# Optimization experiments

Hardware: AMD Instinct MI355X
Metric: run time of the kernel (lower is better)

The kernel has to match this reference:

```python
import jax, jax.numpy as jnp
from jax import lax
import numpy as np

B, L, D = 8, 2048, 512
Q, K = 8, 2048


def setup_inputs() -> dict:
    key = jax.random.key(0)
    kx, kc = jax.random.split(key)
    x = jax.random.normal(kx, (B, L, D), dtype=jnp.float32)
    codebooks = jax.random.normal(kc, (Q, K, D), dtype=jnp.float32)  # Q stacked [K, D] embedding tables
    return {"x": x, "codebooks": codebooks}


def reference(x, codebooks):
    # Residual VQ: at each level, nearest-codeword lookup on the residual.
    # cdist argmin == squared-distance argmin: ||r||^2 - 2 r.c + ||c||^2.
    cb_sq = jnp.sum(codebooks * codebooks, axis=-1)  # [Q, K]

    def step(residual, level):
        cb, cb2 = level  # [K, D], [K]
        r2 = jnp.sum(residual * residual, axis=-1, keepdims=True)  # [B, L, 1]
        dots = jnp.einsum('bld,kd->blk', residual, cb)  # [B, L, K]
        dist2 = r2 - 2.0 * dots + cb2  # [B, L, K]
        idx = jnp.argmin(dist2, axis=-1)  # [B, L]
        quant = cb[idx]  # [B, L, D] gather
        return residual - quant, (idx, quant)

    _, (indices, quants) = lax.scan(step, x, (codebooks, cb_sq))
    quantized = jnp.sum(quants, axis=0)  # [B, L, D]
    indices = jnp.moveaxis(indices, 0, 1)  # [B, Q, L] (torch.stack(dim=1))
    return indices, quantized
```

## Files before the change

kernel.cpp:

```cpp
#include <hip/hip_runtime.h>

#define BB 8
#define LL 2048
#define DD 512
#define QQ 8
#define KK 2048
#define MM (BB*LL)

#define NTILES 16

typedef __attribute__((ext_vector_type(8))) short short8;
typedef __attribute__((ext_vector_type(4))) float f32x4;

#define GLDS(src, dst) __builtin_amdgcn_global_load_lds( \
    (const __attribute__((address_space(1))) void*)(src), \
    (__attribute__((address_space(3))) void*)(dst), 16, 0, 0)

#define BARX()  asm volatile("s_barrier" ::: "memory")
#define WAIT0() asm volatile("s_waitcnt vmcnt(0)" ::: "memory")

__device__ __forceinline__ ushort f2bf(float f) {
    uint u = __float_as_uint(f);
    u += 0x7FFFu + ((u >> 16) & 1u);
    return (ushort)(u >> 16);
}

__global__ __launch_bounds__(256) void cb2_kernel(const float* __restrict__ cb,
                                                  float* __restrict__ cb2) {
    int row  = blockIdx.x * 4 + (threadIdx.x >> 6);
    int lane = threadIdx.x & 63;
    const float* r = cb + (size_t)row * DD + lane * 8;
    float4 a = *(const float4*)r;
    float4 b = *(const float4*)(r + 4);
    float s = a.x*a.x + a.y*a.y + a.z*a.z + a.w*a.w
            + b.x*b.x + b.y*b.y + b.z*b.z + b.w*b.w;
    #pragma unroll
    for (int off = 32; off >= 1; off >>= 1) s += __shfl_xor(s, off);
    if (lane == 0) cb2[row] = s;
}

__global__ __launch_bounds__(256) void bprep_kernel(const float* __restrict__ cbq,
                                                    short8* __restrict__ bh2) {
    const int wid  = threadIdx.x >> 6;
    const int lane = threadIdx.x & 63;
    const int col  = blockIdx.x * 4 + wid;
    const float* src = cbq + (size_t)col * DD + lane * 8;
    float4 v0 = *(const float4*)src;
    float4 v1 = *(const float4*)(src + 4);
    short8 h;
    h[0] = (short)f2bf(v0.x); h[1] = (short)f2bf(v0.y);
    h[2] = (short)f2bf(v0.z); h[3] = (short)f2bf(v0.w);
    h[4] = (short)f2bf(v1.x); h[5] = (short)f2bf(v1.y);
    h[6] = (short)f2bf(v1.z); h[7] = (short)f2bf(v1.w);
    bh2[(size_t)col * 64 + lane] = h;
}

__global__ __launch_bounds__(256) void aprep0_kernel(const float* __restrict__ x,
                                                     float* __restrict__ resid,
                                                     short8* __restrict__ ah) {
    const int wid  = threadIdx.x >> 6;
    const int lane = threadIdx.x & 63;
    const int row  = blockIdx.x * 4 + wid;
    const float* src = x + (size_t)row * DD + lane * 8;
    float4 v0 = *(const float4*)src;
    float4 v1 = *(const float4*)(src + 4);
    float* dst = resid + (size_t)row * DD + lane * 8;
    *(float4*)dst       = v0;
    *(float4*)(dst + 4) = v1;
    short8 h;
    h[0] = (short)f2bf(v0.x); h[1] = (short)f2bf(v0.y);
    h[2] = (short)f2bf(v0.z); h[3] = (short)f2bf(v0.w);
    h[4] = (short)f2bf(v1.x); h[5] = (short)f2bf(v1.y);
    h[6] = (short)f2bf(v1.z); h[7] = (short)f2bf(v1.w);
    ah[(size_t)row * 64 + lane] = h;
}

__global__ __launch_bounds__(512, 2) void gemm_argmin_kernel(
    const short8* __restrict__ ah,
    const short8* __restrict__ bh2,
    const float*  __restrict__ cb2q,
    float*        __restrict__ blockv1,
    uint4*        __restrict__ blockmask,
    float W)
{
    __shared__ char smemc[131072];

    const int id  = blockIdx.x;
    const int xcd = id & 7;
    const int s   = id >> 3;
    const int nt  = s & 7;
    const int mt  = xcd * 8 + (s >> 3);

    const int tid  = threadIdx.x;
    const int wid  = tid >> 6;
    const int lane = tid & 63;
    const int wr   = wid >> 2;
    const int wcn  = wid & 3;
    const int l15  = lane & 15, l4 = lane >> 4;

    f32x4 acc[4][8];
    #pragma unroll
    for (int n = 0; n < 4; n++)
        #pragma unroll
        for (int m = 0; m < 8; m++) acc[n][m] = (f32x4){0.f, 0.f, 0.f, 0.f};

    const char* aSrc = (const char*)ah  + ((size_t)mt << 18);
    const char* bSrc = (const char*)bh2 + ((size_t)nt << 18);

    #define STAGEQ(tt, bufn, p) do { \
        int g_ = (p) * 512 + tid; \
        int rL_ = g_ >> 3, st_ = g_ & 7; \
        int k_ = st_ ^ (rL_ & 7); \
        char* db_ = smemc + (bufn) * 65536 + ((p) * 512 + wid * 64) * 16; \
        GLDS(aSrc + (size_t)rL_ * 1024 + (tt) * 128 + k_ * 16, db_); \
        GLDS(bSrc + (size_t)rL_ * 1024 + (tt) * 128 + k_ * 16, db_ + 32768); \
    } while (0)

    short8 af[4][2], bf[4][2];

    #define LDA(mh) do { \
        _Pragma("unroll") for (int mm = 0; mm < 4; mm++) \
        _Pragma("unroll") for (int ks = 0; ks < 2; ks++) { \
            int rL_ = wr * 128 + ((mh) * 4 + mm) * 16 + l15; \
            int c_ = ks * 4 + l4; \
            af[mm][ks] = *(const short8*)(smemc + ab + rL_ * 128 + ((c_ ^ (rL_ & 7)) << 4)); \
        } } while (0)

    #define LDBALL() do { \
        _Pragma("unroll") for (int nn = 0; nn < 4; nn++) \
        _Pragma("unroll") for (int ks = 0; ks < 2; ks++) { \
            int cL_ = wcn * 64 + nn * 16 + l15; \
            int c_ = ks * 4 + l4; \
            bf[nn][ks] = *(const short8*)(smemc + ab + 32768 + cL_ * 128 + ((c_ ^ (cL_ & 7)) << 4)); \
        } } while (0)

    #define PH(mh) do { \
        __builtin_amdgcn_s_setprio(1); \
        _Pragma("unroll") for (int ks = 0; ks < 2; ks++) \
        _Pragma("unroll") for (int nn = 0; nn < 4; nn++) \
        _Pragma("unroll") for (int mm = 0; mm < 4; mm++) \
            acc[nn][(mh)*4+mm] = __builtin_amdgcn_mfma_f32_16x16x32_bf16( \
                bf[nn][ks], af[mm][ks], acc[nn][(mh)*4+mm], 0, 0, 0); \
        __builtin_amdgcn_s_setprio(0); \
    } while (0)

    STAGEQ(0, 0, 0); STAGEQ(0, 0, 1); STAGEQ(0, 0, 2); STAGEQ(0, 0, 3);
    WAIT0();
    BARX();

    for (int t = 0; t < 8; t++) {
        const uint ab = (uint)(t & 1) * 65536u;
        const int nbuf = (t & 1) ^ 1;
        if (t < 7) { STAGEQ(t + 1, nbuf, 0); STAGEQ(t + 1, nbuf, 1);
                     STAGEQ(t + 1, nbuf, 2); STAGEQ(t + 1, nbuf, 3); }
        LDBALL();
        LDA(0);
        PH(0);
        LDA(1);
        PH(1);
        if (t < 7) WAIT0();
        BARX();
    }

    float* halfmin = (float*)smemc;
    uint2* maskS   = (uint2*)(smemc + 4096);

    f32x4 c2v[4];
    #pragma unroll
    for (int n = 0; n < 4; n++)
        c2v[n] = *(const f32x4*)&cb2q[nt * 256 + wcn * 64 + n * 16 + (l4 << 2)];

    #pragma unroll
    for (int m = 0; m < 8; m++) {
        float v = 3.4e38f;
        #pragma unroll
        for (int n = 0; n < 4; n++)
            #pragma unroll
            for (int r = 0; r < 4; r++)
                v = fminf(v, fmaf(-2.f, acc[n][m][r], c2v[n][r]));
        v = fminf(v, __shfl_xor(v, 16));
        v = fminf(v, __shfl_xor(v, 32));
        if (l4 == 0) halfmin[(wr * 128 + m * 16 + l15) * 4 + wcn] = v;
    }
    __syncthreads();

    #pragma unroll
    for (int m = 0; m < 8; m++) {
        int rL = wr * 128 + m * 16 + l15;
        int pb = wcn & 2;
        float vt = fminf(halfmin[rL * 4 + pb], halfmin[rL * 4 + pb + 1]);
        float thrm = vt + W;
        uint blo = 0, bhi = 0;
        #pragma unroll
        for (int n = 0; n < 4; n++)
            #pragma unroll
            for (int r = 0; r < 4; r++) {
                float d = fmaf(-2.f, acc[n][m][r], c2v[n][r]);
                int bit = n * 16 + (l4 << 2) + r;
                if (d < thrm) { if (bit < 32) blo |= 1u << bit; else bhi |= 1u << (bit - 32); }
            }
        blo |= __shfl_xor(blo, 16); bhi |= __shfl_xor(bhi, 16);
        blo |= __shfl_xor(blo, 32); bhi |= __shfl_xor(bhi, 32);
        if (l4 == 0) maskS[rL * 4 + wcn] = make_uint2(blo, bhi);
    }
    __syncthreads();

    {
        int T = tid >> 8, rL = tid & 255;
        float vt = fminf(halfmin[rL * 4 + T * 2], halfmin[rL * 4 + T * 2 + 1]);
        uint2 lo = maskS[rL * 4 + T * 2], hi = maskS[rL * 4 + T * 2 + 1];
        size_t o = (size_t)(nt * 2 + T) * MM + mt * 256 + rL;
        blockv1[o] = vt;
        blockmask[o] = make_uint4(lo.x, lo.y, hi.x, hi.y);
    }
    #undef STAGEQ
    #undef LDA
    #undef LDBALL
    #undef PH
}

__global__ __launch_bounds__(256) void crru_kernel(
    const float*  __restrict__ blockv1,
    const uint4*  __restrict__ blockmask,
    const float*  __restrict__ cbq,
    const float*  __restrict__ cb2q,
    const float*  __restrict__ xin,
    float*        __restrict__ resid,
    float*        __restrict__ idx_out,
    short8*       __restrict__ ah,
    int q, float W)
{
    __shared__ float rs[4][DD];
    const int wid  = threadIdx.x >> 6;
    const int lane = threadIdx.x & 63;
    const int row  = blockIdx.x * 4 + wid;
    const int grp  = lane >> 4, gl = lane & 15;

    float v1 = 3.4e38f;
    uint4 mk = make_uint4(0, 0, 0, 0);
    if (lane < NTILES) {
        size_t o = (size_t)lane * MM + row;
        v1 = blockv1[o];
        mk = blockmask[o];
    }

    float* rrow = resid + (size_t)row * DD + lane * 8;
    float4 r0 = *(const float4*)rrow;
    float4 r1 = *(const float4*)(rrow + 4);
    *(float4*)&rs[wid][lane * 8]     = r0;
    *(float4*)&rs[wid][lane * 8 + 4] = r1;

    float g1 = v1;
    #pragma unroll
    for (int off = 32; off >= 1; off >>= 1) g1 = fminf(g1, __shfl_xor(g1, off));
    const float thr = g1 + W;

    unsigned long long act = __ballot((lane < NTILES) && (v1 < thr));

    float be = 3.4e38f; int bk = 0x7FFFFFFF;
    const float* rsw = rs[wid];

    auto eval4 = [&](int k0, int k1, int k2, int k3) {
        int kg = (grp == 0) ? k0 : (grp == 1) ? k1 : (grp == 2) ? k2 : k3;
        float d = 0.f;
        if (kg >= 0) {
            const float* cp = cbq + (size_t)kg * DD + gl * 32;
            const float* rp = rsw + gl * 32;
            #pragma unroll
            for (int j = 0; j < 8; j++) {
                float4 c = *(const float4*)(cp + j * 4);
                float4 r = *(const float4*)(rp + j * 4);
                d = fmaf(r.x, c.x, d); d = fmaf(r.y, c.y, d);
                d = fmaf(r.z, c.z, d); d = fmaf(r.w, c.w, d);
            }
        }
        #pragma unroll
        for (int off = 8; off >= 1; off >>= 1) d += __shfl_xor(d, off);
        #pragma unroll
        for (int g = 0; g < 4; g++) {
            float dg = __shfl(d, g * 16);
            int kg2 = (g == 0) ? k0 : (g == 1) ? k1 : (g == 2) ? k2 : k3;
            if (kg2 >= 0) {
                float e = fmaf(-2.f, dg, cb2q[kg2]);
                if (e < be || (e == be && kg2 < bk)) { be = e; bk = kg2; }
            }
        }
    };

    while (act) {
        int tile = __ffsll(act) - 1; act &= act - 1;
        uint m0 = __shfl((int)mk.x, tile), m1 = __shfl((int)mk.y, tile);
        uint m2 = __shfl((int)mk.z, tile), m3 = __shfl((int)mk.w, tile);
        unsigned long long lo = ((unsigned long long)m1 << 32) | m0;
        unsigned long long hi = ((unsigned long long)m3 << 32) | m2;
        int base = tile * 128;
        while (lo | hi) {
            int c0 = -1, c1 = -1, c2 = -1, c3 = -1;
            #define POP1(dst) \
                if (lo) { int b = __ffsll(lo) - 1; lo &= lo - 1; dst = base + b; } \
                else if (hi) { int b = __ffsll(hi) - 1; hi &= hi - 1; dst = base + 64 + b; }
            POP1(c0) POP1(c1) POP1(c2) POP1(c3)
            #undef POP1
            eval4(c0, c1, c2, c3);
        }
    }
    const int winner = bk;

    if (lane == 0) {
        int b = row >> 11, l = row & (LL - 1);
        idx_out[((size_t)b * QQ + q) * LL + l] = (float)winner;
    }

    const float* cw = cbq + (size_t)winner * DD + lane * 8;
    float4 c0 = *(const float4*)cw;
    float4 c1 = *(const float4*)(cw + 4);
    float4 n0 = make_float4(r0.x - c0.x, r0.y - c0.y, r0.z - c0.z, r0.w - c0.w);
    float4 n1 = make_float4(r1.x - c1.x, r1.y - c1.y, r1.z - c1.z, r1.w - c1.w);

    if (q < QQ - 1) {
        *(float4*)rrow       = n0;
        *(float4*)(rrow + 4) = n1;
        short8 h;
        h[0] = (short)f2bf(n0.x); h[1] = (short)f2bf(n0.y);
        h[2] = (short)f2bf(n0.z); h[3] = (short)f2bf(n0.w);
        h[4] = (short)f2bf(n1.x); h[5] = (short)f2bf(n1.y);
        h[6] = (short)f2bf(n1.z); h[7] = (short)f2bf(n1.w);
        ah[(size_t)row * 64 + lane] = h;
    } else {
        const float* xw = xin + (size_t)row * DD + lane * 8;
        float4 x0 = *(const float4*)xw;
        float4 x1 = *(const float4*)(xw + 4);
        *(float4*)rrow       = make_float4(x0.x - n0.x, x0.y - n0.y, x0.z - n0.z, x0.w - n0.w);
        *(float4*)(rrow + 4) = make_float4(x1.x - n1.x, x1.y - n1.y, x1.z - n1.z, x1.w - n1.w);
    }
}

extern "C" void kernel_launch(void* const* d_in, const int* in_sizes, int n_in,
                              void* d_out, int out_size, void* d_ws, size_t ws_size,
                              hipStream_t stream) {
    (void)in_sizes; (void)n_in; (void)out_size; (void)ws_size;
    const float* x  = (const float*)d_in[0];
    const float* cb = (const float*)d_in[1];
    float* out = (float*)d_out;

    float* idx_out = out;
    float* resid   = out + (size_t)BB * QQ * LL;

    char* w = (char*)d_ws;
    float*  cb2       = (float*)(w);
    float*  blockv1   = (float*)(w + 0x10000);
    uint4*  blockmask = (uint4*)(w + 0x110000);
    short8* ah        = (short8*)(w + 0x510000);
    short8* bh2       = (short8*)(w + 0x1510000);

    cb2_kernel<<<QQ * KK / 4, 256, 0, stream>>>(cb, cb2);
    aprep0_kernel<<<MM / 4, 256, 0, stream>>>(x, resid, ah);

    for (int q = 0; q < QQ; q++) {
        const float* cbq = cb + (size_t)q * KK * DD;
        const float* c2q = cb2 + (size_t)q * KK;
        const float W = 2.0f + 0.3f * q;

        bprep_kernel<<<KK / 4, 256, 0, stream>>>(cbq, bh2);

        gemm_argmin_kernel<<<512, 512, 0, stream>>>(ah, bh2, c2q,
                                                    blockv1, blockmask, W);

        crru_kernel<<<MM / 4, 256, 0, stream>>>(blockv1, blockmask, cbq, c2q, x,
                                                resid, idx_out, ah, q, W);
    }
}
```

Measured before the change: 517.1 us.

## Hoist codebook bf16 conversion out of the loop and give each GEMM block two M tiles

The bf16 conversion of all eight codebooks now runs once up front into a larger workspace buffer, instead of one conversion kernel per level. The GEMM/argmin kernel now processes two consecutive 256-row M tiles per block with a continuous double-buffered pipeline across both. It runs the epilogue for the first tile mid-loop, which halves the grid to 256 blocks. This removes per-level launches and may reduce tail and startup cost, at the price of a larger LDS footprint and a longer serial block that needs more workspace.

Measured after the change: 648.6 us. +25.4%, slower.

```diff
diff --git a/kernel.cpp b/kernel.cpp
--- a/kernel.cpp
+++ b/kernel.cpp
@@ -39,12 +39,12 @@
     if (lane == 0) cb2[row] = s;
 }
 
-__global__ __launch_bounds__(256) void bprep_kernel(const float* __restrict__ cbq,
-                                                    short8* __restrict__ bh2) {
+__global__ __launch_bounds__(256) void bprep_kernel(const float* __restrict__ cb,
+                                                    short8* __restrict__ bh2all) {
     const int wid  = threadIdx.x >> 6;
     const int lane = threadIdx.x & 63;
     const int col  = blockIdx.x * 4 + wid;
-    const float* src = cbq + (size_t)col * DD + lane * 8;
+    const float* src = cb + (size_t)col * DD + lane * 8;
     float4 v0 = *(const float4*)src;
     float4 v1 = *(const float4*)(src + 4);
     short8 h;
@@ -52,7 +52,7 @@
     h[2] = (short)f2bf(v0.z); h[3] = (short)f2bf(v0.w);
     h[4] = (short)f2bf(v1.x); h[5] = (short)f2bf(v1.y);
     h[6] = (short)f2bf(v1.z); h[7] = (short)f2bf(v1.w);
-    bh2[(size_t)col * 64 + lane] = h;
+    bh2all[(size_t)col * 64 + lane] = h;
 }
 
 __global__ __launch_bounds__(256) void aprep0_kernel(const float* __restrict__ x,
@@ -77,19 +77,19 @@
 
 __global__ __launch_bounds__(512, 2) void gemm_argmin_kernel(
     const short8* __restrict__ ah,
-    const short8* __restrict__ bh2,
+    const short8* __restrict__ bh2q,
     const float*  __restrict__ cb2q,
     float*        __restrict__ blockv1,
     uint4*        __restrict__ blockmask,
     float W)
 {
-    __shared__ char smemc[131072];
+    __shared__ char smemc[147456];
 
     const int id  = blockIdx.x;
     const int xcd = id & 7;
     const int s   = id >> 3;
     const int nt  = s & 7;
-    const int mt  = xcd * 8 + (s >> 3);
+    const int mt0 = xcd * 8 + (s >> 3) * 2;
 
     const int tid  = threadIdx.x;
     const int wid  = tid >> 6;
@@ -104,16 +104,21 @@
         #pragma unroll
         for (int m = 0; m < 8; m++) acc[n][m] = (f32x4){0.f, 0.f, 0.f, 0.f};
 
-    const char* aSrc = (const char*)ah  + ((size_t)mt << 18);
-    const char* bSrc = (const char*)bh2 + ((size_t)nt << 18);
-
-    #define STAGEQ(tt, bufn, p) do { \
+    const char* aS0  = (const char*)ah + ((size_t)mt0 << 18);
+    const char* aS1  = aS0 + (1 << 18);
+    const char* bSrc = (const char*)bh2q + ((size_t)nt << 18);
+
+    #define STAGEQ(abase, tt, bufn, p) do { \
         int g_ = (p) * 512 + tid; \
         int rL_ = g_ >> 3, st_ = g_ & 7; \
         int k_ = st_ ^ (rL_ & 7); \
         char* db_ = smemc + (bufn) * 65536 + ((p) * 512 + wid * 64) * 16; \
-        GLDS(aSrc + (size_t)rL_ * 1024 + (tt) * 128 + k_ * 16, db_); \
+        GLDS((abase) + (size_t)rL_ * 1024 + (tt) * 128 + k_ * 16, db_); \
         GLDS(bSrc + (size_t)rL_ * 1024 + (tt) * 128 + k_ * 16, db_ + 32768); \
+    } while (0)
+    #define STAGE4(abase, tt, bufn) do { \
+        STAGEQ(abase, tt, bufn, 0); STAGEQ(abase, tt, bufn, 1); \
+        STAGEQ(abase, tt, bufn, 2); STAGEQ(abase, tt, bufn, 3); \
     } while (0)
 
     short8 af[4][2], bf[4][2];
@@ -144,79 +149,87 @@
         __builtin_amdgcn_s_setprio(0); \
     } while (0)
 
-    STAGEQ(0, 0, 0); STAGEQ(0, 0, 1); STAGEQ(0, 0, 2); STAGEQ(0, 0, 3);
+    float* halfmin = (float*)(smemc + 131072);
+    uint2* maskS   = (uint2*)(smemc + 131072 + 4096);
+
+    f32x4 c2v[4];
+    #pragma unroll
+    for (int n = 0; n < 4; n++)
+        c2v[n] = *(const f32x4*)&cb2q[nt * 256 + wcn * 64 + n * 16 + (l4 << 2)];
+
+    #define EPI(mtx) do { \
+        _Pragma("unroll") for (int m = 0; m < 8; m++) { \
+            float v = 3.4e38f; \
+            _Pragma("unroll") for (int n = 0; n < 4; n++) \
+            _Pragma("unroll") for (int r = 0; r < 4; r++) \
+                v = fminf(v, fmaf(-2.f, acc[n][m][r], c2v[n][r])); \
+            v = fminf(v, __shfl_xor(v, 16)); \
+            v = fminf(v, __shfl_xor(v, 32)); \
+            if (l4 == 0) halfmin[(wr * 128 + m * 16 + l15) * 4 + wcn] = v; \
+        } \
+        __syncthreads(); \
+        _Pragma("unroll") for (int m = 0; m < 8; m++) { \
+            int rL = wr * 128 + m * 16 + l15; \
+            int pb = wcn & 2; \
+            float vt = fminf(halfmin[rL * 4 + pb], halfmin[rL * 4 + pb + 1]); \
+            float thrm = vt + W; \
+            uint blo = 0, bhi = 0; \
+            _Pragma("unroll") for (int n = 0; n < 4; n++) \
+            _Pragma("unroll") for (int r = 0; r < 4; r++) { \
+                float d = fmaf(-2.f, acc[n][m][r], c2v[n][r]); \
+                int bit = n * 16 + (l4 << 2) + r; \
+                if (d < thrm) { if (bit < 32) blo |= 1u << bit; else bhi |= 1u << (bit - 32); } \
+            } \
+            blo |= __shfl_xor(blo, 16); bhi |= __shfl_xor(bhi, 16); \
+            blo |= __shfl_xor(blo, 32); bhi |= __shfl_xor(bhi, 32); \
+            if (l4 == 0) maskS[rL * 4 + wcn] = make_uint2(blo, bhi); \
+        } \
+        __syncthreads(); \
+        { \
+            int T = tid >> 8, rL = tid & 255; \
+            float vt = fminf(halfmin[rL * 4 + T * 2], halfmin[rL * 4 + T * 2 + 1]); \
+            uint2 lo = maskS[rL * 4 + T * 2], hi = maskS[rL * 4 + T * 2 + 1]; \
+            size_t o = (size_t)(nt * 2 + T) * MM + (size_t)(mtx) * 256 + rL; \
+            blockv1[o] = vt; \
+            blockmask[o] = make_uint4(lo.x, lo.y, hi.x, hi.y); \
+        } \
+    } while (0)
+
+    STAGE4(aS0, 0, 0);
     WAIT0();
     BARX();
 
-    for (int t = 0; t < 8; t++) {
-        const uint ab = (uint)(t & 1) * 65536u;
-        const int nbuf = (t & 1) ^ 1;
-        if (t < 7) { STAGEQ(t + 1, nbuf, 0); STAGEQ(t + 1, nbuf, 1);
-                     STAGEQ(t + 1, nbuf, 2); STAGEQ(t + 1, nbuf, 3); }
+    for (int vt = 0; vt < 16; vt++) {
+        const uint ab = (uint)(vt & 1) * 65536u;
+        const int nbuf = (vt & 1) ^ 1;
+        if (vt < 15) {
+            int nv = vt + 1;
+            STAGE4((nv < 8 ? aS0 : aS1), nv & 7, nbuf);
+        }
         LDBALL();
         LDA(0);
         PH(0);
         LDA(1);
         PH(1);
-        if (t < 7) WAIT0();
+        if (vt < 15) WAIT0();
         BARX();
-    }
-
-    float* halfmin = (float*)smemc;
-    uint2* maskS   = (uint2*)(smemc + 4096);
-
-    f32x4 c2v[4];
-    #pragma unroll
-    for (int n = 0; n < 4; n++)
-        c2v[n] = *(const f32x4*)&cb2q[nt * 256 + wcn * 64 + n * 16 + (l4 << 2)];
-
-    #pragma unroll
-    for (int m = 0; m < 8; m++) {
-        float v = 3.4e38f;
-        #pragma unroll
-        for (int n = 0; n < 4; n++)
+        if (vt == 7) {
+            EPI(mt0);
             #pragma unroll
-            for (int r = 0; r < 4; r++)
-                v = fminf(v, fmaf(-2.f, acc[n][m][r], c2v[n][r]));
-        v = fminf(v, __shfl_xor(v, 16));
-        v = fminf(v, __shfl_xor(v, 32));
-        if (l4 == 0) halfmin[(wr * 128 + m * 16 + l15) * 4 + wcn] = v;
-    }
-    __syncthreads();
-
-    #pragma unroll
-    for (int m = 0; m < 8; m++) {
-        int rL = wr * 128 + m * 16 + l15;
-        int pb = wcn & 2;
-        float vt = fminf(halfmin[rL * 4 + pb], halfmin[rL * 4 + pb + 1]);
-        float thrm = vt + W;
-        uint blo = 0, bhi = 0;
-        #pragma unroll
-        for (int n = 0; n < 4; n++)
-            #pragma unroll
-            for (int r = 0; r < 4; r++) {
-                float d = fmaf(-2.f, acc[n][m][r], c2v[n][r]);
-                int bit = n * 16 + (l4 << 2) + r;
-                if (d < thrm) { if (bit < 32) blo |= 1u << bit; else bhi |= 1u << (bit - 32); }
-            }
-        blo |= __shfl_xor(blo, 16); bhi |= __shfl_xor(bhi, 16);
-        blo |= __shfl_xor(blo, 32); bhi |= __shfl_xor(bhi, 32);
-        if (l4 == 0) maskS[rL * 4 + wcn] = make_uint2(blo, bhi);
-    }
-    __syncthreads();
-
-    {
-        int T = tid >> 8, rL = tid & 255;
-        float vt = fminf(halfmin[rL * 4 + T * 2], halfmin[rL * 4 + T * 2 + 1]);
-        uint2 lo = maskS[rL * 4 + T * 2], hi = maskS[rL * 4 + T * 2 + 1];
-        size_t o = (size_t)(nt * 2 + T) * MM + mt * 256 + rL;
-        blockv1[o] = vt;
-        blockmask[o] = make_uint4(lo.x, lo.y, hi.x, hi.y);
-    }
+            for (int n = 0; n < 4; n++)
+                #pragma unroll
+                for (int m = 0; m < 8; m++) acc[n][m] = (f32x4){0.f, 0.f, 0.f, 0.f};
+            __syncthreads();
+        }
+    }
+    EPI(mt0 + 1);
+
     #undef STAGEQ
+    #undef STAGE4
     #undef LDA
     #undef LDBALL
     #undef PH
+    #undef EPI
 }
 
 __global__ __launch_bounds__(256) void crru_kernel(
@@ -351,19 +364,19 @@
     float*  blockv1   = (float*)(w + 0x10000);
     uint4*  blockmask = (uint4*)(w + 0x110000);
     short8* ah        = (short8*)(w + 0x510000);
-    short8* bh2       = (short8*)(w + 0x1510000);
+    short8* bh2all    = (short8*)(w + 0x1510000);
 
     cb2_kernel<<<QQ * KK / 4, 256, 0, stream>>>(cb, cb2);
+    bprep_kernel<<<QQ * KK / 4, 256, 0, stream>>>(cb, bh2all);
     aprep0_kernel<<<MM / 4, 256, 0, stream>>>(x, resid, ah);
 
     for (int q = 0; q < QQ; q++) {
-        const float* cbq = cb + (size_t)q * KK * DD;
-        const float* c2q = cb2 + (size_t)q * KK;
+        const float* cbq  = cb + (size_t)q * KK * DD;
+        const float* c2q  = cb2 + (size_t)q * KK;
+        const short8* bhq = bh2all + (size_t)q * KK * 64;
         const float W = 2.0f + 0.3f * q;
 
-        bprep_kernel<<<KK / 4, 256, 0, stream>>>(cbq, bh2);
-
-        gemm_argmin_kernel<<<512, 512, 0, stream>>>(ah, bh2, c2q,
+        gemm_argmin_kernel<<<256, 512, 0, stream>>>(ah, bhq, c2q,
                                                     blockv1, blockmask, W);
 
         crru_kernel<<<MM / 4, 256, 0, stream>>>(blockv1, blockmask, cbq, c2q, x,
```
